# Kernel optimization log

Measured on AMD Instinct MI355X. Metric: run time of the kernel, lower is better.

The kernel has to match this reference:

```python
import jax, jax.numpy as jnp
import numpy as np

N = 100_000      # nodes
E = 1_600_000    # edges (avg degree 16)
EP = 500_000     # pos/neg decode edges each
IN, H, OUT = 256, 128, 64


def setup_inputs() -> dict:
    key = jax.random.key(0)
    ks = jax.random.split(key, 8)
    x = jax.random.normal(ks[0], (N, IN), dtype=jnp.float32)
    edge_index = jax.random.randint(ks[1], (2, E), 0, N, dtype=jnp.int32)
    pos_edge_index = jax.random.randint(ks[2], (2, EP), 0, N, dtype=jnp.int32)
    neg_edge_index = jax.random.randint(ks[3], (2, EP), 0, N, dtype=jnp.int32)
    W1 = jax.random.normal(ks[4], (IN, H), dtype=jnp.float32) * (1.0 / np.sqrt(IN))
    b1 = jnp.zeros((H,), dtype=jnp.float32)
    W2 = jax.random.normal(ks[5], (H, OUT), dtype=jnp.float32) * (1.0 / np.sqrt(H))
    b2 = jnp.zeros((OUT,), dtype=jnp.float32)
    return dict(x=x, edge_index=edge_index, pos_edge_index=pos_edge_index,
                neg_edge_index=neg_edge_index, W1=W1, b1=b1, W2=W2, b2=b2)


def _gcn_conv(x, src, dst, norm, W, b, n_nodes):
    # PyG GCNConv: linear transform, then normalized scatter-add aggregation
    h = x @ W                              # [N, out]
    msg = h[src] * norm[:, None]           # gather + scale, [E+N, out]
    agg = jax.ops.segment_sum(msg, dst, num_segments=n_nodes)
    return agg + b


def reference(x, edge_index, pos_edge_index, neg_edge_index, W1, b1, W2, b2):
    n = x.shape[0]
    loops = jnp.arange(n, dtype=edge_index.dtype)
    src = jnp.concatenate([edge_index[0], loops])   # add self-loops (GCNConv default)
    dst = jnp.concatenate([edge_index[1], loops])
    # symmetric normalization D^{-1/2} (A+I) D^{-1/2}
    deg = jax.ops.segment_sum(jnp.ones_like(src, dtype=x.dtype), dst, num_segments=n)
    dinv = jnp.where(deg > 0, jax.lax.rsqrt(jnp.maximum(deg, 1e-12)), 0.0)
    norm = dinv[src] * dinv[dst]
    # encode
    h = jax.nn.relu(_gcn_conv(x, src, dst, norm, W1, b1, n))
    z = _gcn_conv(h, src, dst, norm, W2, b2, n)
    # decode: edge score = <z_u, z_v> over pos+neg edges
    ei = jnp.concatenate([pos_edge_index, neg_edge_index], axis=-1)
    return (z[ei[0]] * z[ei[1]]).sum(axis=-1)   # [2*EP]
```

## Files before the change

### kernel.cpp

```cpp
#include <hip/hip_runtime.h>


typedef __attribute__((ext_vector_type(8))) short short8;
typedef __attribute__((ext_vector_type(4))) float f32x4;

#define BUK_SHIFT 7
#define BUK_NODES 128

__global__ __launch_bounds__(256) void b_hist_k(const int* __restrict__ dst, int E,
                                                int nbuk, int* __restrict__ bhist) {
  __shared__ int h[1024];
  for (int i = threadIdx.x; i < nbuk; i += 256) h[i] = 0;
  __syncthreads();
  for (int i = blockIdx.x * 256 + threadIdx.x; i < E; i += gridDim.x * 256)
    atomicAdd(&h[dst[i] >> BUK_SHIFT], 1);
  __syncthreads();
  for (int i = threadIdx.x; i < nbuk; i += 256) {
    int c = h[i];
    if (c) atomicAdd(&bhist[i], c);
  }
}

__global__ __launch_bounds__(256) void b_scan_k(const int* __restrict__ bhist,
                                                int nbuk, int* __restrict__ bbase,
                                                int* __restrict__ bcur) {
  __shared__ int arr[256];
  const int t = threadIdx.x;
  const int per = (nbuk + 255) / 256;
  const int start = t * per;
  const int end = min(start + per, nbuk);
  int s = 0;
  for (int i = start; i < end; ++i) s += bhist[i];
  arr[t] = s;
  __syncthreads();
  for (int off = 1; off < 256; off <<= 1) {
    int v = (t >= off) ? arr[t - off] : 0;
    __syncthreads();
    arr[t] += v;
    __syncthreads();
  }
  int run = arr[t] - s;
  for (int i = start; i < end; ++i) {
    bbase[i] = run;
    bcur[i] = run;
    run += bhist[i];
  }
  if (t == 255) bbase[nbuk] = arr[255];
}

__global__ __launch_bounds__(256) void b_scatter_k(const int* __restrict__ src,
                                                   const int* __restrict__ dst, int E,
                                                   int nbuk, int* __restrict__ bcur,
                                                   int* __restrict__ ebuf) {
  __shared__ int lh[1024];
  __shared__ int lc[1024];
  const int base = blockIdx.x * 8192;
  if (base >= E) return;
  const int end = min(base + 8192, E);
  for (int i = threadIdx.x; i < nbuk; i += 256) lh[i] = 0;
  __syncthreads();
  for (int i = base + threadIdx.x; i < end; i += 256)
    atomicAdd(&lh[dst[i] >> BUK_SHIFT], 1);
  __syncthreads();
  for (int i = threadIdx.x; i < nbuk; i += 256) {
    int c = lh[i];
    lc[i] = c ? atomicAdd(&bcur[i], c) : 0;
  }
  __syncthreads();
  for (int i = base + threadIdx.x; i < end; i += 256) {
    int d = dst[i];
    int pos = atomicAdd(&lc[d >> BUK_SHIFT], 1);
    ebuf[pos] = src[i] | ((d & (BUK_NODES - 1)) << 17);
  }
}

__global__ __launch_bounds__(128) void b_build_k(const int* __restrict__ ebuf,
                                                 const int* __restrict__ bbase, int n,
                                                 int nbuk, float* __restrict__ dinv,
                                                 int* __restrict__ rowptr,
                                                 int* __restrict__ csr) {
  __shared__ int cnt[BUK_NODES];
  __shared__ int pre[BUK_NODES];
  __shared__ int cur[BUK_NODES];
  const int b = blockIdx.x, t = threadIdx.x;
  cnt[t] = 0;
  __syncthreads();
  const int beg = bbase[b], end = bbase[b + 1];
  for (int i = beg + t; i < end; i += 128) atomicAdd(&cnt[ebuf[i] >> 17], 1);
  __syncthreads();
  const int c = cnt[t];
  pre[t] = c;
  __syncthreads();
  for (int off = 1; off < 128; off <<= 1) {
    int v = (t >= off) ? pre[t - off] : 0;
    __syncthreads();
    pre[t] += v;
    __syncthreads();
  }
  const int base = beg + pre[t] - c;
  cur[t] = base;
  const int node = (b << BUK_SHIFT) + t;
  if (node < n) {
    rowptr[node] = base;
    dinv[node] = rsqrtf((float)(c + 1));
  }
  if (b == 0 && t == 0) rowptr[n] = bbase[nbuk];
  __syncthreads();
  for (int i = beg + t; i < end; i += 128) {
    int e = ebuf[i];
    int pos = atomicAdd(&cur[e >> 17], 1);
    csr[pos] = e & 0x1FFFF;
  }
}

__global__ __launch_bounds__(256) void split_w_k(const float* __restrict__ W, int K,
                                                 int N,
                                                 unsigned short* __restrict__ hi,
                                                 unsigned short* __restrict__ lo) {
  const int idx = blockIdx.x * 256 + threadIdx.x;
  if (idx >= K * N) return;
  const int k = idx / N, c = idx - k * N;
  const float a = W[idx];
  const unsigned u = __float_as_uint(a);
  const unsigned short h = (unsigned short)(u >> 16);
  const float l = a - __uint_as_float(u & 0xFFFF0000u);
  const unsigned short lb = (unsigned short)(__float_as_uint(l) >> 16);
  hi[(size_t)c * K + k] = h;
  lo[(size_t)c * K + k] = lb;
}

template <int BN>
__global__ __launch_bounds__(256) void gemm_mfma(
    const float* __restrict__ A, const unsigned short* __restrict__ Bthi,
    const unsigned short* __restrict__ Btlo, float* __restrict__ C,
    const float* __restrict__ rowscale, int M, int K) {
  constexpr int BM = 64, BK = 32;
  constexpr int NT = BN / 16;
  constexpr int LD = 40;
  __shared__ unsigned short Ahi[BM * LD];
  __shared__ unsigned short Alo[BM * LD];
  __shared__ unsigned short Bhi[BN * LD];
  __shared__ unsigned short Blo[BN * LD];
  const int tid = threadIdx.x;
  const int lane = tid & 63;
  const int wave = tid >> 6;
  const int rowBase = blockIdx.x * BM;

  f32x4 acc[NT];
#pragma unroll
  for (int c = 0; c < NT; ++c) acc[c] = (f32x4){0.f, 0.f, 0.f, 0.f};

  const int sr = tid >> 2;
  const int sk = (tid & 3) * 8;
  const int arow = wave * 16 + (lane & 15);
  const int akb = (lane >> 4) * 8;

  for (int k0 = 0; k0 < K; k0 += BK) {
    {
      const int gr = rowBase + sr;
      float4 v0 = make_float4(0.f, 0.f, 0.f, 0.f);
      float4 v1 = make_float4(0.f, 0.f, 0.f, 0.f);
      if (gr < M) {
        const float* p = A + (size_t)gr * K + k0 + sk;
        v0 = *reinterpret_cast<const float4*>(p);
        v1 = *reinterpret_cast<const float4*>(p + 4);
      }
      const float vv[8] = {v0.x, v0.y, v0.z, v0.w, v1.x, v1.y, v1.z, v1.w};
      short8 hv, lv;
#pragma unroll
      for (int i = 0; i < 8; ++i) {
        const unsigned u = __float_as_uint(vv[i]);
        hv[i] = (short)(u >> 16);
        const float l = vv[i] - __uint_as_float(u & 0xFFFF0000u);
        lv[i] = (short)(__float_as_uint(l) >> 16);
      }
      *reinterpret_cast<short8*>(&Ahi[sr * LD + sk]) = hv;
      *reinterpret_cast<short8*>(&Alo[sr * LD + sk]) = lv;
    }
    for (int i = tid; i < BN * 2; i += 256) {
      const int col = i >> 1;
      const int kk = (i & 1) * 16;
      const size_t gofs = (size_t)col * K + k0 + kk;
      *reinterpret_cast<short8*>(&Bhi[col * LD + kk]) =
          *reinterpret_cast<const short8*>(&Bthi[gofs]);
      *reinterpret_cast<short8*>(&Bhi[col * LD + kk + 8]) =
          *reinterpret_cast<const short8*>(&Bthi[gofs + 8]);
      *reinterpret_cast<short8*>(&Blo[col * LD + kk]) =
          *reinterpret_cast<const short8*>(&Btlo[gofs]);
      *reinterpret_cast<short8*>(&Blo[col * LD + kk + 8]) =
          *reinterpret_cast<const short8*>(&Btlo[gofs + 8]);
    }
    __syncthreads();
    const short8 fa_hi = *reinterpret_cast<const short8*>(&Ahi[arow * LD + akb]);
    const short8 fa_lo = *reinterpret_cast<const short8*>(&Alo[arow * LD + akb]);
#pragma unroll
    for (int c = 0; c < NT; ++c) {
      const int bofs = (c * 16 + (lane & 15)) * LD + akb;
      const short8 fb_hi = *reinterpret_cast<const short8*>(&Bhi[bofs]);
      const short8 fb_lo = *reinterpret_cast<const short8*>(&Blo[bofs]);
      acc[c] = __builtin_amdgcn_mfma_f32_16x16x32_bf16(fa_hi, fb_hi, acc[c], 0, 0, 0);
      acc[c] = __builtin_amdgcn_mfma_f32_16x16x32_bf16(fa_lo, fb_hi, acc[c], 0, 0, 0);
      acc[c] = __builtin_amdgcn_mfma_f32_16x16x32_bf16(fa_hi, fb_lo, acc[c], 0, 0, 0);
    }
    __syncthreads();
  }
  const int crow = rowBase + wave * 16 + (lane >> 4) * 4;
  float sc[4];
#pragma unroll
  for (int j = 0; j < 4; ++j) sc[j] = (crow + j < M) ? rowscale[crow + j] : 0.f;
#pragma unroll
  for (int c = 0; c < NT; ++c) {
#pragma unroll
    for (int j = 0; j < 4; ++j) {
      const int gr = crow + j;
      if (gr < M) C[(size_t)gr * BN + c * 16 + (lane & 15)] = acc[c][j] * sc[j];
    }
  }
}

__global__ __launch_bounds__(256) void agg128_gemm2_k(
    const float* __restrict__ g1, const int* __restrict__ rowptr,
    const int* __restrict__ csr, const float* __restrict__ dinv,
    const float* __restrict__ bias, const unsigned short* __restrict__ W2thi,
    const unsigned short* __restrict__ W2tlo, float* __restrict__ g2, int n) {
  constexpr int LD2 = 136;
  __shared__ unsigned short Hhi[16 * LD2];
  __shared__ unsigned short Hlo[16 * LD2];
  const int tid = threadIdx.x;
  const int lane = tid & 63;
  const int wave = tid >> 6;
  const int half = lane >> 5;
  const int nb = blockIdx.x * 16;

  const size_t col = (size_t)(lane & 31) * 4;
#pragma unroll
  for (int it = 0; it < 4; ++it) {
    const int row = wave * 4 + it;
    const int node = nb + row;
    float4 r = make_float4(0.f, 0.f, 0.f, 0.f);
    if (node < n) {
      const float dd = dinv[node];
      const int beg = rowptr[node];
      const int end = rowptr[node + 1];
      float4 acc = make_float4(0.f, 0.f, 0.f, 0.f);
      int e = beg;
      for (; e + 8 <= end; e += 8) {
        const int s0 = csr[e + 0 + half];
        const int s1 = csr[e + 2 + half];
        const int s2 = csr[e + 4 + half];
        const int s3 = csr[e + 6 + half];
        const float4 v0 = *reinterpret_cast<const float4*>(&g1[(size_t)s0 * 128 + col]);
        const float4 v1 = *reinterpret_cast<const float4*>(&g1[(size_t)s1 * 128 + col]);
        const float4 v2 = *reinterpret_cast<const float4*>(&g1[(size_t)s2 * 128 + col]);
        const float4 v3 = *reinterpret_cast<const float4*>(&g1[(size_t)s3 * 128 + col]);
        acc.x += (v0.x + v1.x) + (v2.x + v3.x);
        acc.y += (v0.y + v1.y) + (v2.y + v3.y);
        acc.z += (v0.z + v1.z) + (v2.z + v3.z);
        acc.w += (v0.w + v1.w) + (v2.w + v3.w);
      }
      for (; e + 2 <= end; e += 2) {
        const int s = csr[e + half];
        const float4 v = *reinterpret_cast<const float4*>(&g1[(size_t)s * 128 + col]);
        acc.x += v.x;
        acc.y += v.y;
        acc.z += v.z;
        acc.w += v.w;
      }
      if (e < end && half == 0) {
        const int s = csr[e];
        const float4 v = *reinterpret_cast<const float4*>(&g1[(size_t)s * 128 + col]);
        acc.x += v.x;
        acc.y += v.y;
        acc.z += v.z;
        acc.w += v.w;
      }
      acc.x += __shfl_xor(acc.x, 32);
      acc.y += __shfl_xor(acc.y, 32);
      acc.z += __shfl_xor(acc.z, 32);
      acc.w += __shfl_xor(acc.w, 32);
      if (half == 0) {
        const float4 sv = *reinterpret_cast<const float4*>(&g1[(size_t)node * 128 + col]);
        const float4 b = *reinterpret_cast<const float4*>(&bias[col]);
        r.x = fmaxf(dd * (acc.x + sv.x) + b.x, 0.f);
        r.y = fmaxf(dd * (acc.y + sv.y) + b.y, 0.f);
        r.z = fmaxf(dd * (acc.z + sv.z) + b.z, 0.f);
        r.w = fmaxf(dd * (acc.w + sv.w) + b.w, 0.f);
      }
    }
    if (half == 0) {
      const float vv[4] = {r.x, r.y, r.z, r.w};
      ushort4 hv, lv;
      unsigned u0 = __float_as_uint(vv[0]);
      unsigned u1 = __float_as_uint(vv[1]);
      unsigned u2 = __float_as_uint(vv[2]);
      unsigned u3 = __float_as_uint(vv[3]);
      hv.x = (unsigned short)(u0 >> 16);
      hv.y = (unsigned short)(u1 >> 16);
      hv.z = (unsigned short)(u2 >> 16);
      hv.w = (unsigned short)(u3 >> 16);
      lv.x = (unsigned short)(__float_as_uint(vv[0] - __uint_as_float(u0 & 0xFFFF0000u)) >> 16);
      lv.y = (unsigned short)(__float_as_uint(vv[1] - __uint_as_float(u1 & 0xFFFF0000u)) >> 16);
      lv.z = (unsigned short)(__float_as_uint(vv[2] - __uint_as_float(u2 & 0xFFFF0000u)) >> 16);
      lv.w = (unsigned short)(__float_as_uint(vv[3] - __uint_as_float(u3 & 0xFFFF0000u)) >> 16);
      *reinterpret_cast<ushort4*>(&Hhi[row * LD2 + (lane & 31) * 4]) = hv;
      *reinterpret_cast<ushort4*>(&Hlo[row * LD2 + (lane & 31) * 4]) = lv;
    }
  }
  __syncthreads();

  const int ct = wave * 16;
  const int fr = lane & 15;
  const int fk = (lane >> 4) * 8;
  f32x4 acc2 = (f32x4){0.f, 0.f, 0.f, 0.f};
#pragma unroll
  for (int c = 0; c < 4; ++c) {
    const short8 fa_hi = *reinterpret_cast<const short8*>(&Hhi[fr * LD2 + c * 32 + fk]);
    const short8 fa_lo = *reinterpret_cast<const short8*>(&Hlo[fr * LD2 + c * 32 + fk]);
    const size_t bo = (size_t)(ct + fr) * 128 + c * 32 + fk;
    const short8 fb_hi = *reinterpret_cast<const short8*>(&W2thi[bo]);
    const short8 fb_lo = *reinterpret_cast<const short8*>(&W2tlo[bo]);
    acc2 = __builtin_amdgcn_mfma_f32_16x16x32_bf16(fa_hi, fb_hi, acc2, 0, 0, 0);
    acc2 = __builtin_amdgcn_mfma_f32_16x16x32_bf16(fa_lo, fb_hi, acc2, 0, 0, 0);
    acc2 = __builtin_amdgcn_mfma_f32_16x16x32_bf16(fa_hi, fb_lo, acc2, 0, 0, 0);
  }
#pragma unroll
  for (int j = 0; j < 4; ++j) {
    const int node = nb + (lane >> 4) * 4 + j;
    if (node < n) g2[(size_t)node * 64 + ct + fr] = acc2[j] * dinv[node];
  }
}

__global__ __launch_bounds__(256) void agg64_k(const float* __restrict__ g,
                                               const int* __restrict__ rowptr,
                                               const int* __restrict__ csr,
                                               const float* __restrict__ dinv,
                                               const float* __restrict__ bias,
                                               float* __restrict__ hout, int n) {
  const int wid = (blockIdx.x * 256 + threadIdx.x) >> 6;
  if (wid >= n) return;
  const int lane = threadIdx.x & 63;
  const int quad = lane >> 4;
  const size_t col = (size_t)(lane & 15) * 4;
  const float dd = dinv[wid];
  const int beg = rowptr[wid];
  const int end = rowptr[wid + 1];
  float4 acc = make_float4(0.f, 0.f, 0.f, 0.f);
  int e = beg;
  for (; e + 16 <= end; e += 16) {
    const int s0 = csr[e + 0 + quad];
    const int s1 = csr[e + 4 + quad];
    const int s2 = csr[e + 8 + quad];
    const int s3 = csr[e + 12 + quad];
    const float4 v0 = *reinterpret_cast<const float4*>(&g[(size_t)s0 * 64 + col]);
    const float4 v1 = *reinterpret_cast<const float4*>(&g[(size_t)s1 * 64 + col]);
    const float4 v2 = *reinterpret_cast<const float4*>(&g[(size_t)s2 * 64 + col]);
    const float4 v3 = *reinterpret_cast<const float4*>(&g[(size_t)s3 * 64 + col]);
    acc.x += (v0.x + v1.x) + (v2.x + v3.x);
    acc.y += (v0.y + v1.y) + (v2.y + v3.y);
    acc.z += (v0.z + v1.z) + (v2.z + v3.z);
    acc.w += (v0.w + v1.w) + (v2.w + v3.w);
  }
  for (; e + 4 <= end; e += 4) {
    const int s = csr[e + quad];
    const float4 v = *reinterpret_cast<const float4*>(&g[(size_t)s * 64 + col]);
    acc.x += v.x;
    acc.y += v.y;
    acc.z += v.z;
    acc.w += v.w;
  }
  const int r = end - e;
  if (quad < r) {
    const int s = csr[e + quad];
    const float4 v = *reinterpret_cast<const float4*>(&g[(size_t)s * 64 + col]);
    acc.x += v.x;
    acc.y += v.y;
    acc.z += v.z;
    acc.w += v.w;
  }
  acc.x += __shfl_xor(acc.x, 16);
  acc.y += __shfl_xor(acc.y, 16);
  acc.z += __shfl_xor(acc.z, 16);
  acc.w += __shfl_xor(acc.w, 16);
  acc.x += __shfl_xor(acc.x, 32);
  acc.y += __shfl_xor(acc.y, 32);
  acc.z += __shfl_xor(acc.z, 32);
  acc.w += __shfl_xor(acc.w, 32);
  if (quad == 0) {
    const float4 sv = *reinterpret_cast<const float4*>(&g[(size_t)wid * 64 + col]);
    const float4 b = *reinterpret_cast<const float4*>(&bias[col]);
    float4 res;
    res.x = dd * (acc.x + sv.x) + b.x;
    res.y = dd * (acc.y + sv.y) + b.y;
    res.z = dd * (acc.z + sv.z) + b.z;
    res.w = dd * (acc.w + sv.w) + b.w;
    *reinterpret_cast<float4*>(&hout[(size_t)wid * 64 + col]) = res;
  }
}

__global__ __launch_bounds__(256) void decode_k(const int* __restrict__ pos,
                                                const int* __restrict__ neg,
                                                const float* __restrict__ z,
                                                float* __restrict__ out, int EP) {
  const long long t = (long long)blockIdx.x * 256 + threadIdx.x;
  const long long e = t >> 3;
  const int lane = (int)(t & 7);
  if (e >= 2LL * EP) return;
  int u, v;
  if (e < EP) {
    u = pos[e];
    v = pos[EP + e];
  } else {
    u = neg[e - EP];
    v = neg[EP + (e - EP)];
  }
  const float* zu = &z[(size_t)u * 64 + lane * 8];
  const float* zv = &z[(size_t)v * 64 + lane * 8];
  const float4 a0 = *reinterpret_cast<const float4*>(zu);
  const float4 a1 = *reinterpret_cast<const float4*>(zu + 4);
  const float4 b0 = *reinterpret_cast<const float4*>(zv);
  const float4 b1 = *reinterpret_cast<const float4*>(zv + 4);
  float p = a0.x * b0.x + a0.y * b0.y + a0.z * b0.z + a0.w * b0.w +
            a1.x * b1.x + a1.y * b1.y + a1.z * b1.z + a1.w * b1.w;
#pragma unroll
  for (int off = 4; off > 0; off >>= 1) p += __shfl_down(p, off, 8);
  if (lane == 0) out[e] = p;
}


extern "C" void kernel_launch(void* const* d_in, const int* in_sizes, int n_in,
                              void* d_out, int out_size, void* d_ws, size_t ws_size,
                              hipStream_t stream) {
  const float* x = (const float*)d_in[0];
  const int* ei = (const int*)d_in[1];
  const int* pos = (const int*)d_in[2];
  const int* neg = (const int*)d_in[3];
  const float* W1 = (const float*)d_in[4];
  const float* b1 = (const float*)d_in[5];
  const float* W2 = (const float*)d_in[6];
  const float* b2 = (const float*)d_in[7];
  float* out = (float*)d_out;

  const int H = in_sizes[5];
  const int IN = in_sizes[4] / H;
  const int OUT = in_sizes[7];
  const int N = in_sizes[0] / IN;
  const int E = in_sizes[1] / 2;
  const int EP = in_sizes[2] / 2;

  char* ws = (char*)d_ws;
  size_t off = 0;
  auto carve = [&](size_t bytes) -> char* {
    char* p = ws + off;
    off += (bytes + 255) & ~(size_t)255;
    return p;
  };
  const int NBUK = (N + BUK_NODES - 1) >> BUK_SHIFT;

  float* dinvb = (float*)carve((size_t)N * 4);
  int* rowptr = (int*)carve((size_t)(N + 1) * 4);
  int* bhist = (int*)carve((size_t)NBUK * 4);
  int* bbase = (int*)carve((size_t)(NBUK + 1) * 4);
  int* bcur = (int*)carve((size_t)NBUK * 4);
  int* ebuf = (int*)carve((size_t)E * 4);
  int* csr = (int*)carve((size_t)E * 4);
  float* bufA = (float*)carve((size_t)N * H * 4);
  float* bufB = (float*)carve((size_t)N * H * 4);
  unsigned short* w1hi = (unsigned short*)carve((size_t)IN * H * 2);
  unsigned short* w1lo = (unsigned short*)carve((size_t)IN * H * 2);
  unsigned short* w2hi = (unsigned short*)carve((size_t)H * OUT * 2);
  unsigned short* w2lo = (unsigned short*)carve((size_t)H * OUT * 2);
  (void)ws_size;

  const int* srcp = ei;
  const int* dstp = ei + E;

  split_w_k<<<(IN * H + 255) / 256, 256, 0, stream>>>(W1, IN, H, w1hi, w1lo);
  split_w_k<<<(H * OUT + 255) / 256, 256, 0, stream>>>(W2, H, OUT, w2hi, w2lo);

  hipMemsetAsync(bhist, 0, (size_t)NBUK * 4, stream);
  b_hist_k<<<512, 256, 0, stream>>>(dstp, E, NBUK, bhist);
  b_scan_k<<<1, 256, 0, stream>>>(bhist, NBUK, bbase, bcur);
  b_scatter_k<<<(E + 8191) / 8192, 256, 0, stream>>>(srcp, dstp, E, NBUK, bcur, ebuf);
  b_build_k<<<NBUK, 128, 0, stream>>>(ebuf, bbase, N, NBUK, dinvb, rowptr, csr);

  gemm_mfma<128><<<(N + 63) / 64, 256, 0, stream>>>(x, w1hi, w1lo, bufA, dinvb, N, IN);
  agg128_gemm2_k<<<(N + 15) / 16, 256, 0, stream>>>(bufA, rowptr, csr, dinvb, b1,
                                                    w2hi, w2lo, bufB, N);
  agg64_k<<<(N + 3) / 4, 256, 0, stream>>>(bufB, rowptr, csr, dinvb, b2, bufA, N);
  const long long threads = 2LL * EP * 8;
  decode_k<<<(int)((threads + 255) / 256), 256, 0, stream>>>(pos, neg, bufA, out, EP);
}
```

Before: 376.7 us.

## Replace bucket histogram and scan with fixed-capacity buckets; merge weight-split launches

```diff
diff --git a/kernel.cpp b/kernel.cpp
--- a/kernel.cpp
+++ b/kernel.cpp
@@ -6,47 +6,8 @@
 
 #define BUK_SHIFT 7
 #define BUK_NODES 128
-
-__global__ __launch_bounds__(256) void b_hist_k(const int* __restrict__ dst, int E,
-                                                int nbuk, int* __restrict__ bhist) {
-  __shared__ int h[1024];
-  for (int i = threadIdx.x; i < nbuk; i += 256) h[i] = 0;
-  __syncthreads();
-  for (int i = blockIdx.x * 256 + threadIdx.x; i < E; i += gridDim.x * 256)
-    atomicAdd(&h[dst[i] >> BUK_SHIFT], 1);
-  __syncthreads();
-  for (int i = threadIdx.x; i < nbuk; i += 256) {
-    int c = h[i];
-    if (c) atomicAdd(&bhist[i], c);
-  }
-}
-
-__global__ __launch_bounds__(256) void b_scan_k(const int* __restrict__ bhist,
-                                                int nbuk, int* __restrict__ bbase,
-                                                int* __restrict__ bcur) {
-  __shared__ int arr[256];
-  const int t = threadIdx.x;
-  const int per = (nbuk + 255) / 256;
-  const int start = t * per;
-  const int end = min(start + per, nbuk);
-  int s = 0;
-  for (int i = start; i < end; ++i) s += bhist[i];
-  arr[t] = s;
-  __syncthreads();
-  for (int off = 1; off < 256; off <<= 1) {
-    int v = (t >= off) ? arr[t - off] : 0;
-    __syncthreads();
-    arr[t] += v;
-    __syncthreads();
-  }
-  int run = arr[t] - s;
-  for (int i = start; i < end; ++i) {
-    bbase[i] = run;
-    bcur[i] = run;
-    run += bhist[i];
-  }
-  if (t == 255) bbase[nbuk] = arr[255];
-}
+#define CAP_SHIFT 12
+#define BUK_CAP 4096
 
 __global__ __launch_bounds__(256) void b_scatter_k(const int* __restrict__ src,
                                                    const int* __restrict__ dst, int E,
@@ -64,7 +25,7 @@
   __syncthreads();
   for (int i = threadIdx.x; i < nbuk; i += 256) {
     int c = lh[i];
-    lc[i] = c ? atomicAdd(&bcur[i], c) : 0;
+    lc[i] = c ? (i << CAP_SHIFT) + atomicAdd(&bcur[i], c) : 0;
   }
   __syncthreads();
   for (int i = base + threadIdx.x; i < end; i += 256) {
@@ -75,9 +36,10 @@
 }
 
 __global__ __launch_bounds__(128) void b_build_k(const int* __restrict__ ebuf,
-                                                 const int* __restrict__ bbase, int n,
-                                                 int nbuk, float* __restrict__ dinv,
-                                                 int* __restrict__ rowptr,
+                                                 const int* __restrict__ bcur, int n,
+                                                 float* __restrict__ dinv,
+                                                 int* __restrict__ rowbeg,
+                                                 int* __restrict__ rowend,
                                                  int* __restrict__ csr) {
   __shared__ int cnt[BUK_NODES];
   __shared__ int pre[BUK_NODES];
@@ -85,7 +47,8 @@
   const int b = blockIdx.x, t = threadIdx.x;
   cnt[t] = 0;
   __syncthreads();
-  const int beg = bbase[b], end = bbase[b + 1];
+  const int beg = b << CAP_SHIFT;
+  const int end = beg + bcur[b];
   for (int i = beg + t; i < end; i += 128) atomicAdd(&cnt[ebuf[i] >> 17], 1);
   __syncthreads();
   const int c = cnt[t];
@@ -97,14 +60,14 @@
     pre[t] += v;
     __syncthreads();
   }
-  const int base = beg + pre[t] - c;
-  cur[t] = base;
+  const int rb = beg + pre[t] - c;
+  cur[t] = rb;
   const int node = (b << BUK_SHIFT) + t;
   if (node < n) {
-    rowptr[node] = base;
+    rowbeg[node] = rb;
+    rowend[node] = rb + c;
     dinv[node] = rsqrtf((float)(c + 1));
   }
-  if (b == 0 && t == 0) rowptr[n] = bbase[nbuk];
   __syncthreads();
   for (int i = beg + t; i < end; i += 128) {
     int e = ebuf[i];
@@ -113,12 +76,22 @@
   }
 }
 
-__global__ __launch_bounds__(256) void split_w_k(const float* __restrict__ W, int K,
-                                                 int N,
-                                                 unsigned short* __restrict__ hi,
-                                                 unsigned short* __restrict__ lo) {
-  const int idx = blockIdx.x * 256 + threadIdx.x;
-  if (idx >= K * N) return;
+__global__ __launch_bounds__(256) void split_w_k(
+    const float* __restrict__ W1, int K1, int N1, unsigned short* __restrict__ hi1,
+    unsigned short* __restrict__ lo1, const float* __restrict__ W2, int K2, int N2,
+    unsigned short* __restrict__ hi2, unsigned short* __restrict__ lo2) {
+  int idx = blockIdx.x * 256 + threadIdx.x;
+  const int tot1 = K1 * N1;
+  const float* W;
+  unsigned short *hi, *lo;
+  int K, N;
+  if (idx < tot1) {
+    W = W1; hi = hi1; lo = lo1; K = K1; N = N1;
+  } else {
+    idx -= tot1;
+    if (idx >= K2 * N2) return;
+    W = W2; hi = hi2; lo = lo2; K = K2; N = N2;
+  }
   const int k = idx / N, c = idx - k * N;
   const float a = W[idx];
   const unsigned u = __float_as_uint(a);
@@ -219,10 +192,11 @@
 }
 
 __global__ __launch_bounds__(256) void agg128_gemm2_k(
-    const float* __restrict__ g1, const int* __restrict__ rowptr,
-    const int* __restrict__ csr, const float* __restrict__ dinv,
-    const float* __restrict__ bias, const unsigned short* __restrict__ W2thi,
-    const unsigned short* __restrict__ W2tlo, float* __restrict__ g2, int n) {
+    const float* __restrict__ g1, const int* __restrict__ rowbeg,
+    const int* __restrict__ rowend, const int* __restrict__ csr,
+    const float* __restrict__ dinv, const float* __restrict__ bias,
+    const unsigned short* __restrict__ W2thi, const unsigned short* __restrict__ W2tlo,
+    float* __restrict__ g2, int n) {
   constexpr int LD2 = 136;
   __shared__ unsigned short Hhi[16 * LD2];
   __shared__ unsigned short Hlo[16 * LD2];
@@ -240,8 +214,8 @@
     float4 r = make_float4(0.f, 0.f, 0.f, 0.f);
     if (node < n) {
       const float dd = dinv[node];
-      const int beg = rowptr[node];
-      const int end = rowptr[node + 1];
+      const int beg = rowbeg[node];
+      const int end = rowend[node];
       float4 acc = make_float4(0.f, 0.f, 0.f, 0.f);
       int e = beg;
       for (; e + 8 <= end; e += 8) {
@@ -331,7 +305,8 @@
 }
 
 __global__ __launch_bounds__(256) void agg64_k(const float* __restrict__ g,
-                                               const int* __restrict__ rowptr,
+                                               const int* __restrict__ rowbeg,
+                                               const int* __restrict__ rowend,
                                                const int* __restrict__ csr,
                                                const float* __restrict__ dinv,
                                                const float* __restrict__ bias,
@@ -342,8 +317,8 @@
   const int quad = lane >> 4;
   const size_t col = (size_t)(lane & 15) * 4;
   const float dd = dinv[wid];
-  const int beg = rowptr[wid];
-  const int end = rowptr[wid + 1];
+  const int beg = rowbeg[wid];
+  const int end = rowend[wid];
   float4 acc = make_float4(0.f, 0.f, 0.f, 0.f);
   int e = beg;
   for (; e + 16 <= end; e += 16) {
@@ -457,12 +432,11 @@
   const int NBUK = (N + BUK_NODES - 1) >> BUK_SHIFT;
 
   float* dinvb = (float*)carve((size_t)N * 4);
-  int* rowptr = (int*)carve((size_t)(N + 1) * 4);
-  int* bhist = (int*)carve((size_t)NBUK * 4);
-  int* bbase = (int*)carve((size_t)(NBUK + 1) * 4);
+  int* rowbeg = (int*)carve((size_t)N * 4);
+  int* rowend = (int*)carve((size_t)N * 4);
   int* bcur = (int*)carve((size_t)NBUK * 4);
-  int* ebuf = (int*)carve((size_t)E * 4);
-  int* csr = (int*)carve((size_t)E * 4);
+  int* ebuf = (int*)carve((size_t)NBUK * BUK_CAP * 4);
+  int* csr = (int*)carve((size_t)NBUK * BUK_CAP * 4);
   float* bufA = (float*)carve((size_t)N * H * 4);
   float* bufB = (float*)carve((size_t)N * H * 4);
   unsigned short* w1hi = (unsigned short*)carve((size_t)IN * H * 2);
@@ -474,19 +448,18 @@
   const int* srcp = ei;
   const int* dstp = ei + E;
 
-  split_w_k<<<(IN * H + 255) / 256, 256, 0, stream>>>(W1, IN, H, w1hi, w1lo);
-  split_w_k<<<(H * OUT + 255) / 256, 256, 0, stream>>>(W2, H, OUT, w2hi, w2lo);
-
-  hipMemsetAsync(bhist, 0, (size_t)NBUK * 4, stream);
-  b_hist_k<<<512, 256, 0, stream>>>(dstp, E, NBUK, bhist);
-  b_scan_k<<<1, 256, 0, stream>>>(bhist, NBUK, bbase, bcur);
+  split_w_k<<<(IN * H + H * OUT + 255) / 256, 256, 0, stream>>>(
+      W1, IN, H, w1hi, w1lo, W2, H, OUT, w2hi, w2lo);
+
+  hipMemsetAsync(bcur, 0, (size_t)NBUK * 4, stream);
   b_scatter_k<<<(E + 8191) / 8192, 256, 0, stream>>>(srcp, dstp, E, NBUK, bcur, ebuf);
-  b_build_k<<<NBUK, 128, 0, stream>>>(ebuf, bbase, N, NBUK, dinvb, rowptr, csr);
+  b_build_k<<<NBUK, 128, 0, stream>>>(ebuf, bcur, N, dinvb, rowbeg, rowend, csr);
 
   gemm_mfma<128><<<(N + 63) / 64, 256, 0, stream>>>(x, w1hi, w1lo, bufA, dinvb, N, IN);
-  agg128_gemm2_k<<<(N + 15) / 16, 256, 0, stream>>>(bufA, rowptr, csr, dinvb, b1,
-                                                    w2hi, w2lo, bufB, N);
-  agg64_k<<<(N + 3) / 4, 256, 0, stream>>>(bufB, rowptr, csr, dinvb, b2, bufA, N);
+  agg128_gemm2_k<<<(N + 15) / 16, 256, 0, stream>>>(bufA, rowbeg, rowend, csr, dinvb,
+                                                    b1, w2hi, w2lo, bufB, N);
+  agg64_k<<<(N + 3) / 4, 256, 0, stream>>>(bufB, rowbeg, rowend, csr, dinvb, b2,
+                                           bufA, N);
   const long long threads = 2LL * EP * 8;
   decode_k<<<(int)((threads + 255) / 256), 256, 0, stream>>>(pos, neg, bufA, out, EP);
 }
```

Measured after the change: 359.3 us. -4.6%, faster.
